# Kernel tuning notes

Measured on AMD Instinct MI355X. Metric: run time of the kernel, lower is better.

Reference implementation:

```python
import jax, jax.numpy as jnp
import numpy as np

B, T, S, D = 8, 2048, 2048, 256


def setup_inputs() -> dict:
    key = jax.random.key(0)
    k1, k2, k3, k4 = jax.random.split(key, 4)
    source = jax.random.normal(k1, (B, T, D), dtype=jnp.float32)
    memory_bank = jax.random.normal(k2, (B, S, D), dtype=jnp.float32)
    # torch Linear(2*dim, dim, bias=False); stored as [in, out] so y = x @ W_out
    W_out = jax.random.normal(k3, (2 * D, D), dtype=jnp.float32) * 0.05
    memory_lengths = jax.random.randint(k4, (B,), 1, S + 1, dtype=jnp.int64)
    return {"source": source, "memory_bank": memory_bank, "W_out": W_out,
            "memory_lengths": memory_lengths}


def reference(source, memory_bank, W_out, memory_lengths):
    # align[b,t,s] = <source[b,t], memory_bank[b,s]>   (attn_type='dot')
    align = jnp.einsum('btd,bsd->bts', source, memory_bank)
    # sequence mask over source positions
    mask = jnp.arange(S)[None, :] < memory_lengths[:, None]          # [B,S]
    align = jnp.where(mask[:, None, :], align, -jnp.inf)             # [B,T,S]
    # coverage branch (multi-step): exp of shifted scores
    maxes = jnp.max(align, axis=2, keepdims=True)
    exp_score = jnp.exp(align - maxes)                               # [B,T,S]
    # tril-ones bmm == shifted cumulative sum over target steps:
    # penalty[t] = sum_{j<t} exp_score[j] for t>=1, penalty[0] = 1
    penalty = jnp.cumsum(exp_score[:, :-1, :], axis=1)
    penalty = jnp.concatenate(
        [jnp.ones_like(exp_score[:, :1, :]), penalty], axis=1)
    unnormalized = exp_score / (penalty + 1e-20)
    align_vectors = unnormalized / jnp.sum(unnormalized, axis=2, keepdims=True)
    # context and output projection
    c = jnp.einsum('bts,bsd->btd', align_vectors, memory_bank)
    concat_c = jnp.concatenate([c, source], axis=-1)                 # [B,T,2D]
    attn_h = jnp.tanh(concat_c @ W_out)                              # [B,T,D]
    return attn_h, align_vectors
```

## Files before the change

kernel.cpp:

```cpp
#include <hip/hip_runtime.h>
#include <math.h>

#define BN 8
#define TT 2048
#define SS 2048
#define DD 256
#define NSEG 64
#define SEGLEN 32

typedef __attribute__((ext_vector_type(8))) short short8;
typedef __attribute__((ext_vector_type(4))) float floatx4;

__device__ __forceinline__ unsigned short f2bf_rne(float f) {
    unsigned int u = __float_as_uint(f);
    u = (u + 0x7FFFu + ((u >> 16) & 1u)) >> 16;
    return (unsigned short)u;
}
__device__ __forceinline__ float bf2f(unsigned short h) {
    return __uint_as_float(((unsigned int)h) << 16);
}
__device__ __forceinline__ unsigned int fenc(float f) {
    unsigned int b = __float_as_uint(f);
    return (b & 0x80000000u) ? ~b : (b | 0x80000000u);
}
__device__ __forceinline__ float fdec(unsigned int u) {
    return __uint_as_float((u & 0x80000000u) ? (u & 0x7FFFFFFFu) : ~u);
}

__device__ __forceinline__ void async16(const unsigned short* g, unsigned short* l) {
    __builtin_amdgcn_global_load_lds(
        (const __attribute__((address_space(1))) unsigned int*)g,
        (__attribute__((address_space(3))) unsigned int*)l,
        16, 0, 0);
}

__global__ __launch_bounds__(256) void kpre(
    const float* __restrict__ src, const float* __restrict__ mem,
    unsigned short* __restrict__ shi, unsigned short* __restrict__ slo,
    unsigned short* __restrict__ mhirm, unsigned short* __restrict__ mlorm,
    unsigned int* __restrict__ rowmaxU)
{
    if (blockIdx.y == 0 && blockIdx.x < (BN * TT / 256))
        rowmaxU[blockIdx.x * 256 + threadIdx.x] = 0u;
    const float* in; unsigned short *oh, *ol;
    if (blockIdx.y == 0) { in = src; oh = shi; ol = slo; }
    else                 { in = mem; oh = mhirm; ol = mlorm; }
    const size_t base = ((size_t)blockIdx.x * 256 + threadIdx.x) * 8;
    float4 v0 = *(const float4*)(in + base);
    float4 v1 = *(const float4*)(in + base + 4);
    float f[8] = {v0.x, v0.y, v0.z, v0.w, v1.x, v1.y, v1.z, v1.w};
    short8 hv, lv;
#pragma unroll
    for (int j = 0; j < 8; j++) {
        unsigned short h = f2bf_rne(f[j]);
        hv[j] = (short)h;
        lv[j] = (short)f2bf_rne(f[j] - bf2f(h));
    }
    *(short8*)(oh + base) = hv;
    *(short8*)(ol + base) = lv;
}

__global__ __launch_bounds__(256) void k1_mfma(
    const unsigned short* __restrict__ shi, const unsigned short* __restrict__ slo,
    const unsigned short* __restrict__ mhirm, const unsigned short* __restrict__ mlorm,
    const int* __restrict__ lens, float* __restrict__ alignb,
    unsigned int* __restrict__ rowmaxU)
{
    const int b  = blockIdx.z;
    const int len = lens[b];
    const int s0 = blockIdx.x * 128;
    if (s0 >= len) return;
    const int t0 = blockIdx.y * 128;
    const int tid = threadIdx.x;
    const int wave = tid >> 6, lane = tid & 63;
    const int wt = wave & 1, wsb = wave >> 1;
    const int quad = lane >> 4, m = lane & 15;

    __shared__ unsigned short ldsAh[128 * 32];
    __shared__ unsigned short ldsAl[128 * 32];
    __shared__ unsigned short ldsBh[128 * 32];
    __shared__ unsigned short ldsBl[128 * 32];

    const int srow = tid >> 2, sk4 = (tid & 3) * 8;
    const size_t aBase = ((size_t)(b * TT + t0 + srow)) * DD + sk4;
    const size_t bBase = ((size_t)(b * SS + s0 + srow)) * DD + sk4;
    const size_t aBase2 = aBase + (size_t)64 * DD;
    const size_t bBase2 = bBase + (size_t)64 * DD;
    const int lo1 = tid * 8, lo2 = tid * 8 + 2048;

    floatx4 acc[4][4];
#pragma unroll
    for (int i = 0; i < 4; i++)
#pragma unroll
        for (int j = 0; j < 4; j++) acc[i][j] = (floatx4)0.f;

    for (int kc = 0; kc < 8; kc++) {
        const int ko = kc * 32;
        __syncthreads();
        async16(shi   + aBase  + ko, ldsAh + lo1);
        async16(shi   + aBase2 + ko, ldsAh + lo2);
        async16(slo   + aBase  + ko, ldsAl + lo1);
        async16(slo   + aBase2 + ko, ldsAl + lo2);
        async16(mhirm + bBase  + ko, ldsBh + lo1);
        async16(mhirm + bBase2 + ko, ldsBh + lo2);
        async16(mlorm + bBase  + ko, ldsBl + lo1);
        async16(mlorm + bBase2 + ko, ldsBl + lo2);
        __syncthreads();

        short8 Ah[4], Al[4], Bh[4], Bl[4];
#pragma unroll
        for (int f = 0; f < 4; f++) {
            const int ra = (wt * 64 + f * 16 + m) * 32 + quad * 8;
            const int rb = (wsb * 64 + f * 16 + m) * 32 + quad * 8;
            Ah[f] = *(const short8*)&ldsAh[ra];
            Al[f] = *(const short8*)&ldsAl[ra];
            Bh[f] = *(const short8*)&ldsBh[rb];
            Bl[f] = *(const short8*)&ldsBl[rb];
        }
#pragma unroll
        for (int mf = 0; mf < 4; mf++)
#pragma unroll
            for (int nf = 0; nf < 4; nf++) {
                acc[mf][nf] = __builtin_amdgcn_mfma_f32_16x16x32_bf16(
                    Ah[mf], Bh[nf], acc[mf][nf], 0, 0, 0);
                acc[mf][nf] = __builtin_amdgcn_mfma_f32_16x16x32_bf16(
                    Al[mf], Bh[nf], acc[mf][nf], 0, 0, 0);
                acc[mf][nf] = __builtin_amdgcn_mfma_f32_16x16x32_bf16(
                    Ah[mf], Bl[nf], acc[mf][nf], 0, 0, 0);
            }
    }

#pragma unroll
    for (int mf = 0; mf < 4; mf++)
#pragma unroll
        for (int reg = 0; reg < 4; reg++) {
            const int t = t0 + wt * 64 + mf * 16 + quad * 4 + reg;
            float* row = alignb + ((size_t)(b * TT + t)) * SS + s0 + wsb * 64 + m;
#pragma unroll
            for (int nf = 0; nf < 4; nf++)
                row[nf * 16] = acc[mf][nf][reg];
        }

    if (s0 + wsb * 64 < len) {
#pragma unroll
        for (int mf = 0; mf < 4; mf++)
#pragma unroll
            for (int reg = 0; reg < 4; reg++) {
                float mx = -INFINITY;
#pragma unroll
                for (int nf = 0; nf < 4; nf++) {
                    const int col = s0 + wsb * 64 + nf * 16 + m;
                    mx = (col < len) ? fmaxf(mx, acc[mf][nf][reg]) : mx;
                }
#pragma unroll
                for (int off = 1; off < 16; off <<= 1)
                    mx = fmaxf(mx, __shfl_xor(mx, off, 64));
                if (m == 0) {
                    const int t = t0 + wt * 64 + mf * 16 + quad * 4 + reg;
                    atomicMax(&rowmaxU[b * TT + t], fenc(mx));
                }
            }
    }
}

__global__ __launch_bounds__(256) void k3_segsum(
    const float* __restrict__ alignb, const unsigned int* __restrict__ rowmaxU,
    const int* __restrict__ lens, float* __restrict__ segsum)
{
    const int b = blockIdx.z, seg = blockIdx.y;
    const int s = blockIdx.x * 256 + threadIdx.x;
    const size_t oidx = ((size_t)b * NSEG + seg) * SS + s;
    if (s >= lens[b]) { segsum[oidx] = 0.f; return; }
    const float* base = alignb + ((size_t)b * TT + seg * SEGLEN) * SS + s;
    const unsigned int* rmu = rowmaxU + b * TT + seg * SEGLEN;
    float sum = 0.f;
#pragma unroll 4
    for (int r = 0; r < SEGLEN; r++)
        sum += expf(base[(size_t)r * SS] - fdec(rmu[r]));
    segsum[oidx] = sum;
}

__global__ __launch_bounds__(256) void k4_prefix(float* __restrict__ segsum)
{
    const int b = blockIdx.y;
    const int s = blockIdx.x * 256 + threadIdx.x;
    float run = 0.f;
    for (int g = 0; g < NSEG / 8; g++) {
        float v[8];
#pragma unroll
        for (int i = 0; i < 8; i++)
            v[i] = segsum[((size_t)b * NSEG + g * 8 + i) * SS + s];
#pragma unroll
        for (int i = 0; i < 8; i++) {
            segsum[((size_t)b * NSEG + g * 8 + i) * SS + s] = run;
            run += v[i];
        }
    }
}

__global__ __launch_bounds__(256) void k6pre(
    const float* __restrict__ mem, unsigned short* __restrict__ mhi)
{
    const int gid = blockIdx.x * 256 + threadIdx.x;
    const int lane = gid & 63;
    const int dt   = (gid >> 6) & 15;
    const int c    = (gid >> 10) & 63;
    const int b    = gid >> 16;
    const int quad = lane >> 4, n = lane & 15;
    const int s = c * 32 + quad * 8;
    const int d = dt * 16 + n;
    const float* srcp = mem + ((size_t)b * SS + s) * DD + d;
    short8 hi;
#pragma unroll
    for (int j = 0; j < 8; j++)
        hi[j] = (short)f2bf_rne(srcp[(size_t)j * DD]);
    *(short8*)(mhi + (size_t)gid * 8) = hi;
}

__global__ __launch_bounds__(256) void k5_scan_ctx(
    float* __restrict__ alignb, const unsigned int* __restrict__ rowmaxU,
    const float* __restrict__ segsum, const int* __restrict__ lens,
    const unsigned short* __restrict__ mhi, float* __restrict__ cfull)
{
    const int seg = blockIdx.x, b = blockIdx.y;
    const int len = lens[b];
    const int tid = threadIdx.x;
    const int c0 = tid * 8;
    const int lane = tid & 63, wid = tid >> 6;
    const bool anyv = c0 < len;

    __shared__ unsigned short uLds[SEGLEN * SS];
    __shared__ float red[8];

    float psum[8];
    {
        const float* sp = segsum + ((size_t)b * NSEG + seg) * SS + c0;
        float4 a = *(const float4*)sp, c = *(const float4*)(sp + 4);
        psum[0] = a.x; psum[1] = a.y; psum[2] = a.z; psum[3] = a.w;
        psum[4] = c.x; psum[5] = c.y; psum[6] = c.z; psum[7] = c.w;
    }

    float* rowp = alignb + ((size_t)(b * TT + seg * SEGLEN)) * SS + c0;

    float avn[8] = {0.f, 0.f, 0.f, 0.f, 0.f, 0.f, 0.f, 0.f};
    if (anyv) {
        float4 a = *(const float4*)rowp, c = *(const float4*)(rowp + 4);
        avn[0] = a.x; avn[1] = a.y; avn[2] = a.z; avn[3] = a.w;
        avn[4] = c.x; avn[5] = c.y; avn[6] = c.z; avn[7] = c.w;
    }

    for (int r = 0; r < SEGLEN; r++) {
        const int t = seg * SEGLEN + r;
        const float m = fdec(rowmaxU[b * TT + t]);
        float av[8];
#pragma unroll
        for (int j = 0; j < 8; j++) av[j] = avn[j];
        if (anyv && r + 1 < SEGLEN) {
            const float* np = rowp + (size_t)(r + 1) * SS;
            float4 a = *(const float4*)np, c = *(const float4*)(np + 4);
            avn[0] = a.x; avn[1] = a.y; avn[2] = a.z; avn[3] = a.w;
            avn[4] = c.x; avn[5] = c.y; avn[6] = c.z; avn[7] = c.w;
        }
        float u[8], rsum = 0.f;
#pragma unroll
        for (int j = 0; j < 8; j++) {
            float e = (c0 + j < len) ? expf(av[j] - m) : 0.f;
            float div = (t == 0) ? 1.0f : (psum[j] + 1e-20f);
            u[j] = e / div;
            psum[j] += e;
            rsum += u[j];
        }
#pragma unroll
        for (int off = 32; off > 0; off >>= 1)
            rsum += __shfl_down(rsum, off, 64);
        const int pp = (r & 1) * 4;
        if (lane == 0) red[pp + wid] = rsum;
        __syncthreads();
        const float inv = 1.0f / (red[pp] + red[pp + 1] + red[pp + 2] + red[pp + 3]);
        float* wp = rowp + (size_t)r * SS;
        float4 o0 = {u[0] * inv, u[1] * inv, u[2] * inv, u[3] * inv};
        float4 o1 = {u[4] * inv, u[5] * inv, u[6] * inv, u[7] * inv};
        *(float4*)wp = o0;
        *(float4*)(wp + 4) = o1;
        short8 pk;
#pragma unroll
        for (int j = 0; j < 8; j++) pk[j] = (short)f2bf_rne(u[j] * inv);
        const int ub = ((r * SS + c0) * 2) ^ ((r & 7) << 4);
        *(short8*)((char*)uLds + ub) = pk;
    }
    __syncthreads();

    const int quad = lane >> 4, m16 = lane & 15;
    int cmax = (len + 31) >> 5; if (cmax > 64) cmax = 64;
    floatx4 acc[2][4];
#pragma unroll
    for (int i = 0; i < 2; i++)
#pragma unroll
        for (int j = 0; j < 4; j++) acc[i][j] = (floatx4)0.f;

    const unsigned short* mb = mhi + (size_t)b * 64 * 16 * 64 * 8;
#pragma unroll 2
    for (int c = 0; c < cmax; c++) {
        short8 Bf[4];
#pragma unroll
        for (int j = 0; j < 4; j++)
            Bf[j] = *(const short8*)(mb + (((size_t)c * 16 + wid * 4 + j) * 64 + lane) * 8);
        short8 Af[2];
#pragma unroll
        for (int mf = 0; mf < 2; mf++) {
            const int row = mf * 16 + m16;
            const int byte = (row * (SS * 2) + c * 64 + quad * 16) ^ ((row & 7) << 4);
            Af[mf] = *(const short8*)((const char*)uLds + byte);
        }
#pragma unroll
        for (int mf = 0; mf < 2; mf++)
#pragma unroll
            for (int j = 0; j < 4; j++)
                acc[mf][j] = __builtin_amdgcn_mfma_f32_16x16x32_bf16(
                    Af[mf], Bf[j], acc[mf][j], 0, 0, 0);
    }

#pragma unroll
    for (int mf = 0; mf < 2; mf++)
#pragma unroll
        for (int j = 0; j < 4; j++) {
            const int d = wid * 64 + j * 16 + m16;
#pragma unroll
            for (int reg = 0; reg < 4; reg++) {
                const int t = seg * SEGLEN + mf * 16 + quad * 4 + reg;
                cfull[((size_t)(b * TT + t)) * DD + d] = acc[mf][j][reg];
            }
        }
}

__global__ __launch_bounds__(256) void k7_out(
    const float* __restrict__ cfull, const float* __restrict__ src,
    const float* __restrict__ W, float* __restrict__ attn)
{
    const int b = blockIdx.y;
    const int t0 = blockIdx.x * 32;
    const int tid = threadIdx.x;
    const int tx = tid & 63, ty = tid >> 6;

    __shared__ __align__(16) float wT[32][256];
    __shared__ float xT[32][32];

    float4 acc[8];
#pragma unroll
    for (int i = 0; i < 8; i++) acc[i] = make_float4(0.f, 0.f, 0.f, 0.f);

    for (int k0 = 0; k0 < 2 * DD; k0 += 32) {
        __syncthreads();
#pragma unroll
        for (int it = 0; it < 8; it++) {
            int f = tid + it * 256;
            int kr = f >> 6, col = (f & 63) * 4;
            *(float4*)&wT[kr][col] =
                *(const float4*)(W + (size_t)(k0 + kr) * DD + col);
        }
#pragma unroll
        for (int rep = 0; rep < 4; rep++) {
            int idx = tid + rep * 256;
            int r = idx >> 5, c = idx & 31;
            int k = k0 + c;
            float x;
            if (k < DD) {
                x = cfull[((size_t)b * TT + t0 + r) * DD + k];
            } else {
                x = src[((size_t)b * TT + t0 + r) * DD + (k - DD)];
            }
            xT[r][c] = x;
        }
        __syncthreads();
#pragma unroll
        for (int kk = 0; kk < 32; kk++) {
            float4 w4 = *(const float4*)&wT[kk][tx * 4];
#pragma unroll
            for (int r4 = 0; r4 < 8; r4++) {
                float x = xT[ty + r4 * 4][kk];
                acc[r4].x += x * w4.x; acc[r4].y += x * w4.y;
                acc[r4].z += x * w4.z; acc[r4].w += x * w4.w;
            }
        }
    }
#pragma unroll
    for (int r4 = 0; r4 < 8; r4++) {
        const int t = t0 + ty + r4 * 4;
        float4 o;
        o.x = tanhf(acc[r4].x); o.y = tanhf(acc[r4].y);
        o.z = tanhf(acc[r4].z); o.w = tanhf(acc[r4].w);
        *(float4*)(attn + ((size_t)b * TT + t) * DD + tx * 4) = o;
    }
}

extern "C" void kernel_launch(void* const* d_in, const int* in_sizes, int n_in,
                              void* d_out, int out_size, void* d_ws, size_t ws_size,
                              hipStream_t stream)
{
    const float* src  = (const float*)d_in[0];
    const float* mem  = (const float*)d_in[1];
    const float* Wout = (const float*)d_in[2];
    const int*   lens = (const int*)d_in[3];

    float* out    = (float*)d_out;
    float* attn   = out;
    float* alignb = out + (size_t)BN * TT * DD;

    unsigned int* rowmaxU = (unsigned int*)d_ws;
    float* segsum = (float*)(rowmaxU + (size_t)BN * TT);
    unsigned short* mhi = (unsigned short*)(segsum + (size_t)BN * NSEG * SS);
    unsigned short* shi   = mhi + (size_t)BN * SS * DD;
    unsigned short* slo   = shi + (size_t)BN * TT * DD;
    unsigned short* mhirm = slo + (size_t)BN * TT * DD;
    unsigned short* mlorm = mhirm + (size_t)BN * SS * DD;
    float* cfull = (float*)shi;

    kpre<<<dim3(BN * TT * DD / (256 * 8), 2), 256, 0, stream>>>(
        src, mem, shi, slo, mhirm, mlorm, rowmaxU);
    k6pre<<<dim3(BN * 64 * 16 * 64 / 256), 256, 0, stream>>>(mem, mhi);
    k1_mfma<<<dim3(SS / 128, TT / 128, BN), 256, 0, stream>>>(
        shi, slo, mhirm, mlorm, lens, alignb, rowmaxU);
    k3_segsum<<<dim3(SS / 256, NSEG, BN), 256, 0, stream>>>(alignb, rowmaxU, lens, segsum);
    k4_prefix<<<dim3(SS / 256, BN), 256, 0, stream>>>(segsum);
    k5_scan_ctx<<<dim3(NSEG, BN), 256, 0, stream>>>(
        alignb, rowmaxU, segsum, lens, mhi, cfull);
    k7_out<<<dim3(TT / 32, BN), 256, 0, stream>>>(cfull, src, Wout, attn);
}
```

Baseline: 424.1 us.

## Split scan and context GEMM into separate kernels, halve segment length

The fused scan+context kernel, which staged a 128KB bf16 tile in LDS, is split into a scan-only kernel and a standalone context MFMA kernel. The new kernel reads normalized alignment rows from global memory and converts them to bf16 on the fly. Segment length is halved so the scan launches twice as many blocks, and fast exp and reciprocal intrinsics replace expf and division. This is meant to lift the LDS-limited occupancy and serial latency, at the cost of re-reading the alignment matrix from global memory and using slightly less precise arithmetic.

```diff
diff --git a/kernel.cpp b/kernel.cpp
--- a/kernel.cpp
+++ b/kernel.cpp
@@ -5,8 +5,8 @@
 #define TT 2048
 #define SS 2048
 #define DD 256
-#define NSEG 64
-#define SEGLEN 32
+#define NSEG 128
+#define SEGLEN 16
 
 typedef __attribute__((ext_vector_type(8))) short short8;
 typedef __attribute__((ext_vector_type(4))) float floatx4;
@@ -176,7 +176,7 @@
     float sum = 0.f;
 #pragma unroll 4
     for (int r = 0; r < SEGLEN; r++)
-        sum += expf(base[(size_t)r * SS] - fdec(rmu[r]));
+        sum += __expf(base[(size_t)r * SS] - fdec(rmu[r]));
     segsum[oidx] = sum;
 }
 
@@ -217,19 +217,16 @@
     *(short8*)(mhi + (size_t)gid * 8) = hi;
 }
 
-__global__ __launch_bounds__(256) void k5_scan_ctx(
+__global__ __launch_bounds__(256) void k5_scan(
     float* __restrict__ alignb, const unsigned int* __restrict__ rowmaxU,
-    const float* __restrict__ segsum, const int* __restrict__ lens,
-    const unsigned short* __restrict__ mhi, float* __restrict__ cfull)
+    const float* __restrict__ segsum, const int* __restrict__ lens)
 {
     const int seg = blockIdx.x, b = blockIdx.y;
     const int len = lens[b];
-    const int tid = threadIdx.x;
-    const int c0 = tid * 8;
-    const int lane = tid & 63, wid = tid >> 6;
+    const int c0 = threadIdx.x * 8;
+    const int lane = threadIdx.x & 63, wid = threadIdx.x >> 6;
     const bool anyv = c0 < len;
 
-    __shared__ unsigned short uLds[SEGLEN * SS];
     __shared__ float red[8];
 
     float psum[8];
@@ -264,9 +261,9 @@
         float u[8], rsum = 0.f;
 #pragma unroll
         for (int j = 0; j < 8; j++) {
-            float e = (c0 + j < len) ? expf(av[j] - m) : 0.f;
+            float e = (c0 + j < len) ? __expf(av[j] - m) : 0.f;
             float div = (t == 0) ? 1.0f : (psum[j] + 1e-20f);
-            u[j] = e / div;
+            u[j] = e * __builtin_amdgcn_rcpf(div);
             psum[j] += e;
             rsum += u[j];
         }
@@ -282,52 +279,64 @@
         float4 o1 = {u[4] * inv, u[5] * inv, u[6] * inv, u[7] * inv};
         *(float4*)wp = o0;
         *(float4*)(wp + 4) = o1;
-        short8 pk;
-#pragma unroll
-        for (int j = 0; j < 8; j++) pk[j] = (short)f2bf_rne(u[j] * inv);
-        const int ub = ((r * SS + c0) * 2) ^ ((r & 7) << 4);
-        *(short8*)((char*)uLds + ub) = pk;
-    }
-    __syncthreads();
-
-    const int quad = lane >> 4, m16 = lane & 15;
-    int cmax = (len + 31) >> 5; if (cmax > 64) cmax = 64;
+    }
+}
+
+__global__ __launch_bounds__(256, 4) void k6_context(
+    const float* __restrict__ alignb, const unsigned short* __restrict__ mhi,
+    const int* __restrict__ lens, float* __restrict__ cfull)
+{
+    const int b  = blockIdx.x;
+    const int t0 = blockIdx.y * 32;
+    const int tid  = threadIdx.x;
+    const int wave = tid >> 6, lane = tid & 63;
+    const int quad = lane >> 4, m = lane & 15;
+
+    const int len = lens[b];
+    int cmax = (len + 31) >> 5;
+    if (cmax > 64) cmax = 64;
+
     floatx4 acc[2][4];
 #pragma unroll
     for (int i = 0; i < 2; i++)
 #pragma unroll
         for (int j = 0; j < 4; j++) acc[i][j] = (floatx4)0.f;
 
-    const unsigned short* mb = mhi + (size_t)b * 64 * 16 * 64 * 8;
-#pragma unroll 2
+    const float* aBase = alignb + ((size_t)(b * TT + t0 + m)) * SS + quad * 8;
+
     for (int c = 0; c < cmax; c++) {
         short8 Bf[4];
 #pragma unroll
-        for (int j = 0; j < 4; j++)
-            Bf[j] = *(const short8*)(mb + (((size_t)c * 16 + wid * 4 + j) * 64 + lane) * 8);
-        short8 Af[2];
+        for (int j = 0; j < 4; j++) {
+            const int dt = wave * 4 + j;
+            Bf[j] = *(const short8*)(mhi +
+                (((size_t)(b * 64 + c) * 16 + dt) * 64 + lane) * 8);
+        }
 #pragma unroll
         for (int mf = 0; mf < 2; mf++) {
-            const int row = mf * 16 + m16;
-            const int byte = (row * (SS * 2) + c * 64 + quad * 16) ^ ((row & 7) << 4);
-            Af[mf] = *(const short8*)((const char*)uLds + byte);
-        }
-#pragma unroll
-        for (int mf = 0; mf < 2; mf++)
+            const float* ap = aBase + (size_t)(mf * 16) * SS + c * 32;
+            float4 v0 = *(const float4*)ap;
+            float4 v1 = *(const float4*)(ap + 4);
+            union { short8 s; unsigned int u[4]; } pk;
+            pk.u[0] = (__float_as_uint(v0.x) >> 16) | (__float_as_uint(v0.y) & 0xFFFF0000u);
+            pk.u[1] = (__float_as_uint(v0.z) >> 16) | (__float_as_uint(v0.w) & 0xFFFF0000u);
+            pk.u[2] = (__float_as_uint(v1.x) >> 16) | (__float_as_uint(v1.y) & 0xFFFF0000u);
+            pk.u[3] = (__float_as_uint(v1.z) >> 16) | (__float_as_uint(v1.w) & 0xFFFF0000u);
 #pragma unroll
             for (int j = 0; j < 4; j++)
                 acc[mf][j] = __builtin_amdgcn_mfma_f32_16x16x32_bf16(
-                    Af[mf], Bf[j], acc[mf][j], 0, 0, 0);
+                    pk.s, Bf[j], acc[mf][j], 0, 0, 0);
+        }
     }
 
 #pragma unroll
     for (int mf = 0; mf < 2; mf++)
 #pragma unroll
         for (int j = 0; j < 4; j++) {
-            const int d = wid * 64 + j * 16 + m16;
+            const int d = wave * 64 + j * 16 + m;
 #pragma unroll
             for (int reg = 0; reg < 4; reg++) {
-                const int t = seg * SEGLEN + mf * 16 + quad * 4 + reg;
+                const int t = t0 + mf * 16 + quad * 4 + reg;
                 cfull[((size_t)(b * TT + t)) * DD + d] = acc[mf][j][reg];
             }
         }
@@ -422,7 +431,7 @@
         shi, slo, mhirm, mlorm, lens, alignb, rowmaxU);
     k3_segsum<<<dim3(SS / 256, NSEG, BN), 256, 0, stream>>>(alignb, rowmaxU, lens, segsum);
     k4_prefix<<<dim3(SS / 256, BN), 256, 0, stream>>>(segsum);
-    k5_scan_ctx<<<dim3(NSEG, BN), 256, 0, stream>>>(
-        alignb, rowmaxU, segsum, lens, mhi, cfull);
+    k5_scan<<<dim3(NSEG, BN), 256, 0, stream>>>(alignb, rowmaxU, segsum, lens);
+    k6_context<<<dim3(BN, TT / 32), 256, 0, stream>>>(alignb, mhi, lens, cfull);
     k7_out<<<dim3(TT / 32, BN), 256, 0, stream>>>(cfull, src, Wout, attn);
 }
```

Result: no change. 425.4 us (+0.3%).
